# Kernel optimization log

Hardware: AMD Instinct MI355X
Metric: run time of the kernel (lower is better)

## Reference

```python
import jax, jax.numpy as jnp
import numpy as np

DT_RANK = 128
DIM_INNER = 2048
D_STATE = 16
IN_FEATURES = 2048


def setup_inputs() -> dict:
    key = jax.random.key(0)
    ks = jax.random.split(key, 6)
    B, L = 2, 2048
    x = jax.random.normal(ks[0], (B, L, IN_FEATURES), dtype=jnp.float32)
    out_dbc = DT_RANK + 2 * D_STATE
    W_dbc = jax.random.normal(ks[1], (out_dbc, IN_FEATURES), dtype=jnp.float32) / np.sqrt(IN_FEATURES)
    b_dbc = jax.random.normal(ks[2], (out_dbc,), dtype=jnp.float32) * 0.01
    W_dt = jax.random.normal(ks[3], (DIM_INNER, DT_RANK), dtype=jnp.float32) / np.sqrt(DT_RANK)
    b_dt = jax.random.normal(ks[4], (DIM_INNER,), dtype=jnp.float32) * 0.01
    A_log = jnp.log(jnp.tile(jnp.arange(1, D_STATE + 1, dtype=jnp.float32), (DIM_INNER, 1)))
    D = jnp.ones((DIM_INNER,), dtype=jnp.float32)
    return {"x": x, "W_dbc": W_dbc, "b_dbc": b_dbc, "W_dt": W_dt, "b_dt": b_dt, "A_log": A_log, "D": D}


def _scan_combine(e1, e2):
    a1, b1 = e1
    a2, b2 = e2
    return a1 * a2, a2 * b1 + b2


def reference(x, W_dbc, b_dbc, W_dt, b_dt, A_log, D):
    # x: (B, L, Din) with Din == dim_inner
    A = -jnp.exp(A_log)                               # (Din, N)
    deltaBC = x @ W_dbc.T + b_dbc                     # (B, L, dt_rank + 2N)
    delta_lo = deltaBC[..., :DT_RANK]
    Bmat = deltaBC[..., DT_RANK:DT_RANK + D_STATE]    # (B, L, N)
    Cmat = deltaBC[..., DT_RANK + D_STATE:]           # (B, L, N)
    delta = jax.nn.softplus(delta_lo @ W_dt.T + b_dt) # (B, L, Din)
    deltaA = jnp.exp(delta[..., None] * A)            # (B, L, Din, N)
    BX = (delta[..., None] * Bmat[:, :, None, :]) * x[..., None]  # (B, L, Din, N)
    # first-order linear recurrence h_t = deltaA_t * h_{t-1} + BX_t, h_{-1}=0
    _, hs = jax.lax.associative_scan(_scan_combine, (deltaA, BX), axis=1)
    y = jnp.einsum("blds,bls->bld", hs, Cmat) + D * x
    return y
```

## Files before the change

### kernel.cpp

```cpp
#include <hip/hip_runtime.h>
#include <hip/hip_bf16.h>
#include <math.h>

#define BATCH  2
#define LSEQ   2048
#define FEAT   2048
#define DINNER 2048
#define DSTATE 16
#define DTRANK 128
#define NDBC   160
#define NCHUNK 64
#define LCHUNK (LSEQ / NCHUNK)
#define BL     (BATCH * LSEQ)
#define KSPLIT 8
#define KCH    (FEAT / KSPLIT)
#define KSUB   64
#define BSTRIDE 72

typedef __attribute__((ext_vector_type(8))) short bf16x8;
typedef __attribute__((ext_vector_type(4))) short bf16x4;
typedef __attribute__((ext_vector_type(4))) float floatx4;

#if __has_builtin(__builtin_amdgcn_exp2f)
#define EXP2F(x) __builtin_amdgcn_exp2f(x)
#else
#define EXP2F(x) exp2f(x)
#endif
#if __has_builtin(__builtin_amdgcn_logf)
#define LOG2F(x) __builtin_amdgcn_logf(x)
#else
#define LOG2F(x) __log2f(x)
#endif

__device__ inline float softplus_fast(float v) {
    float e = EXP2F(-fabsf(v) * 1.4426950408889634f);
    return fmaxf(v, 0.f) + 0.6931471805599453f * LOG2F(1.f + e);
}

__device__ inline void split8(floatx4 a0, floatx4 a1, bf16x8* h, bf16x8* l) {
    union { bf16x8 v; __hip_bfloat16 e[8]; } H, L;
    float v[8] = {a0[0], a0[1], a0[2], a0[3], a1[0], a1[1], a1[2], a1[3]};
#pragma unroll
    for (int i = 0; i < 8; ++i) {
        H.e[i] = __float2bfloat16(v[i]);
        L.e[i] = __float2bfloat16(v[i] - __bfloat162float(H.e[i]));
    }
    *h = H.v; *l = L.v;
}

__global__ __launch_bounds__(256) void split_bf16(const float* __restrict__ src,
                                                  __hip_bfloat16* __restrict__ hi,
                                                  __hip_bfloat16* __restrict__ lo,
                                                  int n8) {
    int t = blockIdx.x * 256 + threadIdx.x;
    if (t >= n8) return;
    const floatx4* s4 = (const floatx4*)(src) + t * 2;
    bf16x8 h, l;
    split8(s4[0], s4[1], &h, &l);
    ((bf16x8*)hi)[t] = h;
    ((bf16x8*)lo)[t] = l;
}

__global__ __launch_bounds__(256) void prep_a2(const float* __restrict__ Alog,
                                               float* __restrict__ A2T) {
    int tid = blockIdx.x * 256 + threadIdx.x;
    int s = tid >> 11;
    int d = tid & (DINNER - 1);
    A2T[s * DINNER + d] = -__expf(Alog[d * DSTATE + s]) * 1.4426950408889634f;
}

__global__ __launch_bounds__(256) void gemm_dbc(
    const float* __restrict__ x,
    const __hip_bfloat16* __restrict__ wh, const __hip_bfloat16* __restrict__ wl,
    float* __restrict__ partial)
{
    __shared__ union {
        struct { __hip_bfloat16 Bh[NDBC * BSTRIDE]; __hip_bfloat16 Bl[NDBC * BSTRIDE]; } s;
        float tile[64 * 164];
    } sm;
    int mt = blockIdx.x, ks = blockIdx.y;
    int t = threadIdx.x;
    int wave = t >> 6, lane = t & 63, lm = lane & 15, q = lane >> 4;
    int m0 = mt * 64;
    int k0 = ks * KCH;
    const float* xrow = x + (size_t)(m0 + wave * 16 + lm) * FEAT;
    floatx4 acc[10];
#pragma unroll
    for (int i = 0; i < 10; ++i) acc[i] = (floatx4){0.f, 0.f, 0.f, 0.f};
    int sr = t >> 3, scb = t & 7;
    for (int kc = 0; kc < KCH; kc += KSUB) {
#pragma unroll
        for (int r = sr; r < NDBC; r += 32) {
            size_t g = (size_t)r * FEAT + k0 + kc + scb * 8;
            *(bf16x8*)&sm.s.Bh[r * BSTRIDE + scb * 8] = *(const bf16x8*)&wh[g];
            *(bf16x8*)&sm.s.Bl[r * BSTRIDE + scb * 8] = *(const bf16x8*)&wl[g];
        }
        __syncthreads();
#pragma unroll
        for (int kk = 0; kk < KSUB; kk += 32) {
            int col = k0 + kc + kk + q * 8;
            floatx4 a0 = *(const floatx4*)(xrow + col);
            floatx4 a1 = *(const floatx4*)(xrow + col + 4);
            bf16x8 ah, al;
            split8(a0, a1, &ah, &al);
#pragma unroll
            for (int nt = 0; nt < 10; ++nt) {
                int boff = (nt * 16 + lm) * BSTRIDE + kk + q * 8;
                bf16x8 bh = *(const bf16x8*)&sm.s.Bh[boff];
                bf16x8 bl = *(const bf16x8*)&sm.s.Bl[boff];
                acc[nt] = __builtin_amdgcn_mfma_f32_16x16x32_bf16(ah, bh, acc[nt], 0, 0, 0);
                acc[nt] = __builtin_amdgcn_mfma_f32_16x16x32_bf16(ah, bl, acc[nt], 0, 0, 0);
                acc[nt] = __builtin_amdgcn_mfma_f32_16x16x32_bf16(al, bh, acc[nt], 0, 0, 0);
            }
        }
        __syncthreads();
    }
#pragma unroll
    for (int nt = 0; nt < 10; ++nt)
#pragma unroll
        for (int i = 0; i < 4; ++i)
            sm.tile[(wave * 16 + q * 4 + i) * 164 + nt * 16 + lm] = acc[nt][i];
    __syncthreads();
#pragma unroll
    for (int it = 0; it < 10; ++it) {
        int idx = it * 256 + t;
        int row = idx / 40, cq = (idx - row * 40) * 4;
        floatx4 v = *(const floatx4*)&sm.tile[row * 164 + cq];
        *(floatx4*)&partial[((size_t)ks * BL + m0 + row) * NDBC + cq] = v;
    }
}

__global__ __launch_bounds__(256) void finalize_dbc(
    const float* __restrict__ partial, const float* __restrict__ bias,
    float* __restrict__ dbcBC, __hip_bfloat16* __restrict__ dhi, __hip_bfloat16* __restrict__ dlo)
{
    int tid = blockIdx.x * 256 + threadIdx.x;
    int m = tid / 40, c4 = tid - m * 40;
    int n = c4 * 4;
    floatx4 s = *(const floatx4*)(bias + n);
#pragma unroll
    for (int ks = 0; ks < KSPLIT; ++ks) {
        floatx4 p = *(const floatx4*)(partial + ((size_t)ks * BL + m) * NDBC + n);
        s = s + p;
    }
    if (c4 < 32) {
        union { bf16x4 v; __hip_bfloat16 e[4]; } H, L;
#pragma unroll
        for (int i = 0; i < 4; ++i) {
            H.e[i] = __float2bfloat16(s[i]);
            L.e[i] = __float2bfloat16(s[i] - __bfloat162float(H.e[i]));
        }
        *(bf16x4*)(dhi + (size_t)m * DTRANK + n) = H.v;
        *(bf16x4*)(dlo + (size_t)m * DTRANK + n) = L.v;
    } else {
        *(floatx4*)(dbcBC + (size_t)m * 32 + (n - 128)) = s;
    }
}

__global__ __launch_bounds__(256) void gemm_dt(
    const __hip_bfloat16* __restrict__ dhi, const __hip_bfloat16* __restrict__ dlo,
    const __hip_bfloat16* __restrict__ wh, const __hip_bfloat16* __restrict__ wl,
    const float* __restrict__ bdt, float* __restrict__ delta)
{
    __shared__ float tile[128 * 68];
    int mt = blockIdx.x, ntb = blockIdx.y;
    int t = threadIdx.x, wave = t >> 6, lane = t & 63, lm = lane & 15, q = lane >> 4;
    int m0 = mt * 128 + wave * 32;
    int n0 = ntb * 64;
    bf16x8 AH[2][4], AL[2][4];
#pragma unroll
    for (int sub = 0; sub < 2; ++sub) {
        const __hip_bfloat16* ah = dhi + (size_t)(m0 + sub * 16 + lm) * DTRANK + q * 8;
        const __hip_bfloat16* al = dlo + (size_t)(m0 + sub * 16 + lm) * DTRANK + q * 8;
#pragma unroll
        for (int kp = 0; kp < 4; ++kp) {
            AH[sub][kp] = *(const bf16x8*)(ah + kp * 32);
            AL[sub][kp] = *(const bf16x8*)(al + kp * 32);
        }
    }
    floatx4 acc[4][2];
#pragma unroll
    for (int i = 0; i < 4; ++i)
#pragma unroll
        for (int j = 0; j < 2; ++j) acc[i][j] = (floatx4){0.f, 0.f, 0.f, 0.f};
#pragma unroll
    for (int nt = 0; nt < 4; ++nt) {
        const __hip_bfloat16* bh = wh + (size_t)(n0 + nt * 16 + lm) * DTRANK + q * 8;
        const __hip_bfloat16* blp = wl + (size_t)(n0 + nt * 16 + lm) * DTRANK + q * 8;
#pragma unroll
        for (int kp = 0; kp < 4; ++kp) {
            bf16x8 bhv = *(const bf16x8*)(bh + kp * 32);
            bf16x8 blv = *(const bf16x8*)(blp + kp * 32);
#pragma unroll
            for (int sub = 0; sub < 2; ++sub) {
                acc[nt][sub] = __builtin_amdgcn_mfma_f32_16x16x32_bf16(AH[sub][kp], bhv, acc[nt][sub], 0, 0, 0);
                acc[nt][sub] = __builtin_amdgcn_mfma_f32_16x16x32_bf16(AH[sub][kp], blv, acc[nt][sub], 0, 0, 0);
                acc[nt][sub] = __builtin_amdgcn_mfma_f32_16x16x32_bf16(AL[sub][kp], bhv, acc[nt][sub], 0, 0, 0);
            }
        }
    }
    int wrow = wave * 32;
#pragma unroll
    for (int nt = 0; nt < 4; ++nt) {
        float bias = bdt[n0 + nt * 16 + lm];
#pragma unroll
        for (int sub = 0; sub < 2; ++sub)
#pragma unroll
            for (int i = 0; i < 4; ++i) {
                float v = acc[nt][sub][i] + bias;
                tile[(wrow + sub * 16 + q * 4 + i) * 68 + nt * 16 + lm] = softplus_fast(v);
            }
    }
    __syncthreads();
#pragma unroll
    for (int it = 0; it < 8; ++it) {
        int idx = it * 256 + t;
        int row = idx >> 4, cq = (idx & 15) * 4;
        floatx4 v = *(const floatx4*)&tile[row * 68 + cq];
        *(floatx4*)&delta[(size_t)(mt * 128 + row) * DINNER + n0 + cq] = v;
    }
}

__global__ __launch_bounds__(256) void scan_partial(
    const float* __restrict__ delta, const float* __restrict__ x,
    const float* __restrict__ dbcBC, const float* __restrict__ A2T,
    float* __restrict__ hA, float* __restrict__ sumd)
{
    __shared__ float BC[LCHUNK * 32];
    int t = threadIdx.x;
    int gtid = blockIdx.x * 256 + t;
    int d = gtid & (DINNER - 1);
    int c = (gtid >> 11) & (NCHUNK - 1);
    int b = gtid >> 17;
    {
        int row = t >> 3, cq = (t & 7) * 4;
        *(floatx4*)&BC[row * 32 + cq] =
            *(const floatx4*)&dbcBC[(size_t)(b * LSEQ + c * LCHUNK + row) * 32 + cq];
    }
    float a2[DSTATE], h[DSTATE];
#pragma unroll
    for (int s = 0; s < DSTATE; ++s) { a2[s] = A2T[s * DINNER + d]; h[s] = 0.f; }
    __syncthreads();
    const float* dp = delta + (size_t)(b * LSEQ + c * LCHUNK) * DINNER + d;
    const float* xp = x + (size_t)(b * LSEQ + c * LCHUNK) * DINNER + d;
    float dl = *dp, xv = *xp, sd = 0.f;
    for (int i = 0; i < LCHUNK - 1; ++i) {
        dp += DINNER; xp += DINNER;
        float dln = *dp, xvn = *xp;
        float du = dl * xv;
        sd += dl;
        const floatx4* Bq = (const floatx4*)&BC[i * 32];
#pragma unroll
        for (int qq = 0; qq < 4; ++qq) {
            floatx4 Bv = Bq[qq];
#pragma unroll
            for (int j = 0; j < 4; ++j) {
                int s = qq * 4 + j;
                h[s] = fmaf(EXP2F(dl * a2[s]), h[s], du * Bv[j]);
            }
        }
        dl = dln; xv = xvn;
    }
    {
        float du = dl * xv;
        sd += dl;
        const floatx4* Bq = (const floatx4*)&BC[(LCHUNK - 1) * 32];
#pragma unroll
        for (int qq = 0; qq < 4; ++qq) {
            floatx4 Bv = Bq[qq];
#pragma unroll
            for (int j = 0; j < 4; ++j) {
                int s = qq * 4 + j;
                h[s] = fmaf(EXP2F(dl * a2[s]), h[s], du * Bv[j]);
            }
        }
    }
    size_t hbase = ((size_t)((b * NCHUNK + c) * 4) * DINNER + d) * 4;
#pragma unroll
    for (int qq = 0; qq < 4; ++qq) {
        floatx4 v = {h[qq * 4], h[qq * 4 + 1], h[qq * 4 + 2], h[qq * 4 + 3]};
        *(floatx4*)&hA[hbase + (size_t)qq * DINNER * 4] = v;
    }
    sumd[(size_t)(b * NCHUNK + c) * DINNER + d] = sd;
}

__global__ __launch_bounds__(256) void scan_combine(
    float* __restrict__ hA, const float* __restrict__ sumd, const float* __restrict__ A2T)
{
    int tid = blockIdx.x * 256 + threadIdx.x;
    int s = tid & 15;
    int d = (tid >> 4) & (DINNER - 1);
    int b = tid >> 15;
    float a2s = A2T[s * DINNER + d];
    int q = s >> 2, e = s & 3;
    size_t hoff = ((size_t)(b * NCHUNK * 4 + q) * DINNER + d) * 4 + e;
    size_t soff = (size_t)(b * NCHUNK) * DINNER + d;
    const size_t hstep = (size_t)16 * DINNER;
    float hin = 0.f;
#pragma unroll
    for (int g = 0; g < NCHUNK / 16; ++g) {
        float sdv[16], hv[16];
#pragma unroll
        for (int k = 0; k < 16; ++k) {
            int cc = g * 16 + k;
            sdv[k] = sumd[soff + (size_t)cc * DINNER];
            hv[k] = hA[hoff + (size_t)cc * hstep];
        }
#pragma unroll
        for (int k = 0; k < 16; ++k) {
            int cc = g * 16 + k;
            hA[hoff + (size_t)cc * hstep] = hin;
            hin = EXP2F(a2s * sdv[k]) * hin + hv[k];
        }
    }
}

__global__ __launch_bounds__(256) void scan_final(
    const float* __restrict__ delta, const float* __restrict__ x,
    const float* __restrict__ dbcBC, const float* __restrict__ A2T,
    const float* __restrict__ hin, const float* __restrict__ Dp,
    float* __restrict__ out)
{
    __shared__ float BC[LCHUNK * 32];
    int t = threadIdx.x;
    int gtid = blockIdx.x * 256 + t;
    int d = gtid & (DINNER - 1);
    int c = (gtid >> 11) & (NCHUNK - 1);
    int b = gtid >> 17;
    {
        int row = t >> 3, cq = (t & 7) * 4;
        *(floatx4*)&BC[row * 32 + cq] =
            *(const floatx4*)&dbcBC[(size_t)(b * LSEQ + c * LCHUNK + row) * 32 + cq];
    }
    float a2[DSTATE], h[DSTATE];
    size_t hbase = ((size_t)((b * NCHUNK + c) * 4) * DINNER + d) * 4;
#pragma unroll
    for (int qq = 0; qq < 4; ++qq) {
        floatx4 v = *(const floatx4*)&hin[hbase + (size_t)qq * DINNER * 4];
#pragma unroll
        for (int j = 0; j < 4; ++j) h[qq * 4 + j] = v[j];
    }
#pragma unroll
    for (int s = 0; s < DSTATE; ++s) a2[s] = A2T[s * DINNER + d];
    float Dd = Dp[d];
    __syncthreads();
    size_t base = (size_t)(b * LSEQ + c * LCHUNK) * DINNER + d;
    const float* dp = delta + base;
    const float* xp = x + base;
    float* op = out + base;
    float dl = *dp, xv = *xp;
    for (int i = 0; i < LCHUNK - 1; ++i) {
        dp += DINNER; xp += DINNER;
        float dln = *dp, xvn = *xp;
        float du = dl * xv;
        float y = 0.f;
        const floatx4* Pq = (const floatx4*)&BC[i * 32];
#pragma unroll
        for (int qq = 0; qq < 4; ++qq) {
            floatx4 Bv = Pq[qq];
            floatx4 Cv = Pq[qq + 4];
#pragma unroll
            for (int j = 0; j < 4; ++j) {
                int s = qq * 4 + j;
                h[s] = fmaf(EXP2F(dl * a2[s]), h[s], du * Bv[j]);
                y = fmaf(h[s], Cv[j], y);
            }
        }
        *op = fmaf(Dd, xv, y);
        op += DINNER;
        dl = dln; xv = xvn;
    }
    {
        float du = dl * xv;
        float y = 0.f;
        const floatx4* Pq = (const floatx4*)&BC[(LCHUNK - 1) * 32];
#pragma unroll
        for (int qq = 0; qq < 4; ++qq) {
            floatx4 Bv = Pq[qq];
            floatx4 Cv = Pq[qq + 4];
#pragma unroll
            for (int j = 0; j < 4; ++j) {
                int s = qq * 4 + j;
                h[s] = fmaf(EXP2F(dl * a2[s]), h[s], du * Bv[j]);
                y = fmaf(h[s], Cv[j], y);
            }
        }
        *op = fmaf(Dd, xv, y);
    }
}

extern "C" void kernel_launch(void* const* d_in, const int* in_sizes, int n_in,
                              void* d_out, int out_size, void* d_ws, size_t ws_size,
                              hipStream_t stream) {
    const float* x    = (const float*)d_in[0];
    const float* Wdbc = (const float*)d_in[1];
    const float* bdbc = (const float*)d_in[2];
    const float* Wdt  = (const float*)d_in[3];
    const float* bdt  = (const float*)d_in[4];
    const float* Alog = (const float*)d_in[5];
    const float* Dp   = (const float*)d_in[6];
    float* out = (float*)d_out;

    char* w = (char*)d_ws;
    __hip_bfloat16* wdbch = (__hip_bfloat16*)w;  w += (size_t)NDBC * FEAT * 2;
    __hip_bfloat16* wdbcl = (__hip_bfloat16*)w;  w += (size_t)NDBC * FEAT * 2;
    __hip_bfloat16* wdth = (__hip_bfloat16*)w;   w += (size_t)DINNER * DTRANK * 2;
    __hip_bfloat16* wdtl = (__hip_bfloat16*)w;   w += (size_t)DINNER * DTRANK * 2;
    float* partial = (float*)w;                  w += (size_t)KSPLIT * BL * NDBC * 4;
    float* dbcBC = (float*)w;                    w += (size_t)BL * 32 * 4;
    __hip_bfloat16* dhi = (__hip_bfloat16*)w;    w += (size_t)BL * DTRANK * 2;
    __hip_bfloat16* dlo = (__hip_bfloat16*)w;    w += (size_t)BL * DTRANK * 2;
    float* delta = (float*)w;                    w += (size_t)BL * DINNER * 4;
    float* A2T = (float*)w;                      w += (size_t)DSTATE * DINNER * 4;
    float* hA = (float*)w;                       w += (size_t)BATCH * NCHUNK * DINNER * DSTATE * 4;
    float* sumd = (float*)w;                     w += (size_t)BATCH * NCHUNK * DINNER * 4;

    hipLaunchKernelGGL(split_bf16, dim3(NDBC * FEAT / 8 / 256), dim3(256), 0, stream,
                       Wdbc, wdbch, wdbcl, NDBC * FEAT / 8);
    hipLaunchKernelGGL(split_bf16, dim3(DINNER * DTRANK / 8 / 256), dim3(256), 0, stream,
                       Wdt, wdth, wdtl, DINNER * DTRANK / 8);
    hipLaunchKernelGGL(prep_a2, dim3((DSTATE * DINNER) / 256), dim3(256), 0, stream, Alog, A2T);
    hipLaunchKernelGGL(gemm_dbc, dim3(BL / 64, KSPLIT), dim3(256), 0, stream,
                       x, wdbch, wdbcl, partial);
    hipLaunchKernelGGL(finalize_dbc, dim3(BL * 40 / 256), dim3(256), 0, stream,
                       partial, bdbc, dbcBC, dhi, dlo);
    hipLaunchKernelGGL(gemm_dt, dim3(BL / 128, DINNER / 64), dim3(256), 0, stream,
                       dhi, dlo, wdth, wdtl, bdt, delta);
    hipLaunchKernelGGL(scan_partial, dim3((BATCH * NCHUNK * DINNER) / 256), dim3(256), 0, stream,
                       delta, x, dbcBC, A2T, hA, sumd);
    hipLaunchKernelGGL(scan_combine, dim3((BATCH * DINNER * DSTATE) / 256), dim3(256), 0, stream,
                       hA, sumd, A2T);
    hipLaunchKernelGGL(scan_final, dim3((BATCH * NCHUNK * DINNER) / 256), dim3(256), 0, stream,
                       delta, x, dbcBC, A2T, hA, Dp, out);
}
```

Before: 211.7 us.

## Merge prep kernels, halve dbc K-split, deepen scan load prefetch

Result: no change. 210.5 us (-0.5%).

```diff
diff --git a/kernel.cpp b/kernel.cpp
--- a/kernel.cpp
+++ b/kernel.cpp
@@ -12,7 +12,7 @@
 #define NCHUNK 64
 #define LCHUNK (LSEQ / NCHUNK)
 #define BL     (BATCH * LSEQ)
-#define KSPLIT 8
+#define KSPLIT 4
 #define KCH    (FEAT / KSPLIT)
 #define KSUB   64
 #define BSTRIDE 72
@@ -48,12 +48,9 @@
     *h = H.v; *l = L.v;
 }
 
-__global__ __launch_bounds__(256) void split_bf16(const float* __restrict__ src,
-                                                  __hip_bfloat16* __restrict__ hi,
-                                                  __hip_bfloat16* __restrict__ lo,
-                                                  int n8) {
-    int t = blockIdx.x * 256 + threadIdx.x;
-    if (t >= n8) return;
+__device__ inline void split_store8(const float* __restrict__ src, int t,
+                                    __hip_bfloat16* __restrict__ hi,
+                                    __hip_bfloat16* __restrict__ lo) {
     const floatx4* s4 = (const floatx4*)(src) + t * 2;
     bf16x8 h, l;
     split8(s4[0], s4[1], &h, &l);
@@ -61,12 +58,24 @@
     ((bf16x8*)lo)[t] = l;
 }
 
-__global__ __launch_bounds__(256) void prep_a2(const float* __restrict__ Alog,
-                                               float* __restrict__ A2T) {
-    int tid = blockIdx.x * 256 + threadIdx.x;
-    int s = tid >> 11;
-    int d = tid & (DINNER - 1);
-    A2T[s * DINNER + d] = -__expf(Alog[d * DSTATE + s]) * 1.4426950408889634f;
+__global__ __launch_bounds__(256) void prep_all(
+    const float* __restrict__ Wdbc, const float* __restrict__ Wdt,
+    const float* __restrict__ Alog,
+    __hip_bfloat16* __restrict__ wdbch, __hip_bfloat16* __restrict__ wdbcl,
+    __hip_bfloat16* __restrict__ wdth, __hip_bfloat16* __restrict__ wdtl,
+    float* __restrict__ A2T)
+{
+    int blk = blockIdx.x;
+    if (blk < 160) {
+        split_store8(Wdbc, blk * 256 + threadIdx.x, wdbch, wdbcl);
+    } else if (blk < 288) {
+        split_store8(Wdt, (blk - 160) * 256 + threadIdx.x, wdth, wdtl);
+    } else {
+        int tid = (blk - 288) * 256 + threadIdx.x;
+        int s = tid >> 11;
+        int d = tid & (DINNER - 1);
+        A2T[s * DINNER + d] = -__expf(Alog[d * DSTATE + s]) * 1.4426950408889634f;
+    }
 }
 
 __global__ __launch_bounds__(256) void gemm_dbc(
@@ -241,12 +250,11 @@
 #pragma unroll
     for (int s = 0; s < DSTATE; ++s) { a2[s] = A2T[s * DINNER + d]; h[s] = 0.f; }
     __syncthreads();
-    const float* dp = delta + (size_t)(b * LSEQ + c * LCHUNK) * DINNER + d;
-    const float* xp = x + (size_t)(b * LSEQ + c * LCHUNK) * DINNER + d;
-    float dl = *dp, xv = *xp, sd = 0.f;
-    for (int i = 0; i < LCHUNK - 1; ++i) {
-        dp += DINNER; xp += DINNER;
-        float dln = *dp, xvn = *xp;
+    int base = (b * LSEQ + c * LCHUNK) * DINNER + d;
+    const float* dp = delta + base;
+    const float* xp = x + base;
+    float sd = 0.f;
+    auto step = [&](int i, float dl, float xv) {
         float du = dl * xv;
         sd += dl;
         const floatx4* Bq = (const floatx4*)&BC[i * 32];
@@ -259,22 +267,17 @@
                 h[s] = fmaf(EXP2F(dl * a2[s]), h[s], du * Bv[j]);
             }
         }
-        dl = dln; xv = xvn;
-    }
-    {
-        float du = dl * xv;
-        sd += dl;
-        const floatx4* Bq = (const floatx4*)&BC[(LCHUNK - 1) * 32];
-#pragma unroll
-        for (int qq = 0; qq < 4; ++qq) {
-            floatx4 Bv = Bq[qq];
-#pragma unroll
-            for (int j = 0; j < 4; ++j) {
-                int s = qq * 4 + j;
-                h[s] = fmaf(EXP2F(dl * a2[s]), h[s], du * Bv[j]);
-            }
-        }
-    }
+    };
+    float dlA = dp[0], xvA = xp[0];
+    float dlB = dp[DINNER], xvB = xp[DINNER];
+    for (int i = 0; i < LCHUNK - 2; ++i) {
+        float dlC = dp[(i + 2) * DINNER];
+        float xvC = xp[(i + 2) * DINNER];
+        step(i, dlA, xvA);
+        dlA = dlB; xvA = xvB; dlB = dlC; xvB = xvC;
+    }
+    step(LCHUNK - 2, dlA, xvA);
+    step(LCHUNK - 1, dlB, xvB);
     size_t hbase = ((size_t)((b * NCHUNK + c) * 4) * DINNER + d) * 4;
 #pragma unroll
     for (int qq = 0; qq < 4; ++qq) {
@@ -344,14 +347,11 @@
     for (int s = 0; s < DSTATE; ++s) a2[s] = A2T[s * DINNER + d];
     float Dd = Dp[d];
     __syncthreads();
-    size_t base = (size_t)(b * LSEQ + c * LCHUNK) * DINNER + d;
+    int base = (b * LSEQ + c * LCHUNK) * DINNER + d;
     const float* dp = delta + base;
     const float* xp = x + base;
     float* op = out + base;
-    float dl = *dp, xv = *xp;
-    for (int i = 0; i < LCHUNK - 1; ++i) {
-        dp += DINNER; xp += DINNER;
-        float dln = *dp, xvn = *xp;
+    auto step = [&](int i, float dl, float xv) {
         float du = dl * xv;
         float y = 0.f;
         const floatx4* Pq = (const floatx4*)&BC[i * 32];
@@ -366,27 +366,18 @@
                 y = fmaf(h[s], Cv[j], y);
             }
         }
-        *op = fmaf(Dd, xv, y);
-        op += DINNER;
-        dl = dln; xv = xvn;
-    }
-    {
-        float du = dl * xv;
-        float y = 0.f;
-        const floatx4* Pq = (const floatx4*)&BC[(LCHUNK - 1) * 32];
-#pragma unroll
-        for (int qq = 0; qq < 4; ++qq) {
-            floatx4 Bv = Pq[qq];
-            floatx4 Cv = Pq[qq + 4];
-#pragma unroll
-            for (int j = 0; j < 4; ++j) {
-                int s = qq * 4 + j;
-                h[s] = fmaf(EXP2F(dl * a2[s]), h[s], du * Bv[j]);
-                y = fmaf(h[s], Cv[j], y);
-            }
-        }
-        *op = fmaf(Dd, xv, y);
-    }
+        op[i * DINNER] = fmaf(Dd, xv, y);
+    };
+    float dlA = dp[0], xvA = xp[0];
+    float dlB = dp[DINNER], xvB = xp[DINNER];
+    for (int i = 0; i < LCHUNK - 2; ++i) {
+        float dlC = dp[(i + 2) * DINNER];
+        float xvC = xp[(i + 2) * DINNER];
+        step(i, dlA, xvA);
+        dlA = dlB; xvA = xvB; dlB = dlC; xvB = xvC;
+    }
+    step(LCHUNK - 2, dlA, xvA);
+    step(LCHUNK - 1, dlB, xvB);
 }
 
 extern "C" void kernel_launch(void* const* d_in, const int* in_sizes, int n_in,
@@ -415,11 +406,8 @@
     float* hA = (float*)w;                       w += (size_t)BATCH * NCHUNK * DINNER * DSTATE * 4;
     float* sumd = (float*)w;                     w += (size_t)BATCH * NCHUNK * DINNER * 4;
 
-    hipLaunchKernelGGL(split_bf16, dim3(NDBC * FEAT / 8 / 256), dim3(256), 0, stream,
-                       Wdbc, wdbch, wdbcl, NDBC * FEAT / 8);
-    hipLaunchKernelGGL(split_bf16, dim3(DINNER * DTRANK / 8 / 256), dim3(256), 0, stream,
-                       Wdt, wdth, wdtl, DINNER * DTRANK / 8);
-    hipLaunchKernelGGL(prep_a2, dim3((DSTATE * DINNER) / 256), dim3(256), 0, stream, Alog, A2T);
+    hipLaunchKernelGGL(prep_all, dim3(416), dim3(256), 0, stream,
+                       Wdbc, Wdt, Alog, wdbch, wdbcl, wdth, wdtl, A2T);
     hipLaunchKernelGGL(gemm_dbc, dim3(BL / 64, KSPLIT), dim3(256), 0, stream,
                        x, wdbch, wdbcl, partial);
     hipLaunchKernelGGL(finalize_dbc, dim3(BL * 40 / 256), dim3(256), 0, stream,
```
